# Kernel tuning notes

Hardware: AMD Instinct MI355X
Metric: run time of the kernel (lower is better)

Reference implementation:

```python
import jax, jax.numpy as jnp
import numpy as np

B, FP, ENC, H, V, SEQ = 512, 4096, 64, 512, 42, 128


def _lin(k, out_d, in_d, scale=0.05):
    kw, kb = jax.random.split(k)
    return (jax.random.normal(kw, (out_d, in_d), jnp.float32) * scale,
            jax.random.normal(kb, (out_d,), jnp.float32) * scale)


def setup_inputs() -> dict:
    key = jax.random.key(0)
    ks = jax.random.split(key, 16)
    inp = {}
    inp["X"] = jax.random.normal(ks[0], (B, FP), jnp.float32)
    inp["y"] = jax.random.normal(ks[1], (B, SEQ, V), jnp.float32)
    inp["eps"] = jax.random.normal(ks[2], (B, ENC), jnp.float32)
    inp["e_fc1w"], inp["e_fc1b"] = _lin(ks[3], 2048, FP, 0.02)
    inp["e_fc2w"], inp["e_fc2b"] = _lin(ks[4], 1024, 2048)
    inp["e_fc3w"], inp["e_fc3b"] = _lin(ks[5], 512, 1024)
    inp["e_fc41w"], inp["e_fc41b"] = _lin(ks[6], ENC, 512)
    inp["e_fc42w"], inp["e_fc42b"] = _lin(ks[7], ENC, 512)
    inp["d_fc1w"], inp["d_fc1b"] = _lin(ks[8], H, ENC)
    inp["d_fc2w"], inp["d_fc2b"] = _lin(ks[9], V, H)
    inp["w_ih0"], inp["b_ih0"] = _lin(ks[10], 3 * H, V)
    inp["w_hh0"], inp["b_hh0"] = _lin(ks[11], 3 * H, H)
    inp["w_ih1"], inp["b_ih1"] = _lin(ks[12], 3 * H, H)
    inp["w_hh1"], inp["b_hh1"] = _lin(ks[13], 3 * H, H)
    return inp


def _gru_cell(x, h, w_ih, w_hh, b_ih, b_hh):
    # PyTorch GRU gate math.
    gi = x @ w_ih.T + b_ih  # [B, 3H]
    gh = h @ w_hh.T + b_hh  # [B, 3H]
    ir, iz, i_n = jnp.split(gi, 3, axis=-1)
    hr, hz, h_n = jnp.split(gh, 3, axis=-1)
    r = jax.nn.sigmoid(ir + hr)
    z = jax.nn.sigmoid(iz + hz)
    n = jnp.tanh(i_n + r * h_n)
    return (1.0 - z) * n + z * h


def reference(X, y, eps, e_fc1w, e_fc1b, e_fc2w, e_fc2b, e_fc3w, e_fc3b,
              e_fc41w, e_fc41b, e_fc42w, e_fc42b, d_fc1w, d_fc1b,
              d_fc2w, d_fc2b, w_ih0, b_ih0, w_hh0, b_hh0,
              w_ih1, b_ih1, w_hh1, b_hh1):
    # --- VAE encoder ---
    h1 = jax.nn.relu(X @ e_fc1w.T + e_fc1b)
    h2 = jax.nn.relu(h1 @ e_fc2w.T + e_fc2b)
    h3 = jax.nn.relu(h2 @ e_fc3w.T + e_fc3b)
    mu = h3 @ e_fc41w.T + e_fc41b
    logvar = h3 @ e_fc42w.T + e_fc42b
    kld = jnp.mean(-0.5 * jnp.sum(1.0 + logvar - mu ** 2 - jnp.exp(logvar), axis=1))
    encoded = eps * jnp.exp(0.5 * logvar) + mu  # reparameterize (eps supplied)

    batch = X.shape[0]
    lat = encoded @ d_fc1w.T + d_fc1b  # [B, H]
    hid0 = jnp.zeros((2, batch, H), X.dtype).at[0].set(lat)
    start = jnp.zeros((V,), X.dtype).at[41].set(1.0)
    x0 = jnp.broadcast_to(start, (batch, V))

    def step(carry, _):
        x, hid = carry
        h_l0 = _gru_cell(x, hid[0], w_ih0, w_hh0, b_ih0, b_hh0)
        h_l1 = _gru_cell(h_l0, hid[1], w_ih1, w_hh1, b_ih1, b_hh1)
        out = h_l1 @ d_fc2w.T + d_fc2b  # [B, V]
        return (out, jnp.stack([h_l0, h_l1])), out

    _, outs = jax.lax.scan(step, (x0, hid0), None, length=SEQ)
    decoded = jnp.transpose(outs, (1, 0, 2))  # [B, SEQ, V]
    return decoded, kld
```

## Files before the change

kernel.cpp:

```cpp
#include <hip/hip_runtime.h>
#include <math.h>

constexpr int kB = 512, kENC = 64, kH = 512, kV = 42, kSEQ = 128;
constexpr int kWPitch = 520;
constexpr int kWRows  = 96;
constexpr int kZPad   = kWRows * kWPitch;
constexpr int kCsAByte = (kZPad + 32) * 2;
constexpr int kLdsBytes = kCsAByte + 30720 + 15360;

typedef __attribute__((ext_vector_type(8))) short bf16x8;
typedef __attribute__((ext_vector_type(4))) float f32x4;
typedef unsigned long long u64;

__device__ __forceinline__ unsigned short f2bf(float x) {
  union { float f; unsigned u; } c; c.f = x;
  unsigned r = c.u + 0x7FFFu + ((c.u >> 16) & 1u);
  return (unsigned short)(r >> 16);
}
__device__ __forceinline__ float sigm(float x) { return 1.f / (1.f + expf(-x)); }

__device__ __forceinline__ void ld_row16(const unsigned short* p, bf16x8 (&r)[16]) {
  asm volatile(
    "global_load_dwordx4 %0, %16, off sc0 sc1\n\t"
    "global_load_dwordx4 %1, %16, off offset:64 sc0 sc1\n\t"
    "global_load_dwordx4 %2, %16, off offset:128 sc0 sc1\n\t"
    "global_load_dwordx4 %3, %16, off offset:192 sc0 sc1\n\t"
    "global_load_dwordx4 %4, %16, off offset:256 sc0 sc1\n\t"
    "global_load_dwordx4 %5, %16, off offset:320 sc0 sc1\n\t"
    "global_load_dwordx4 %6, %16, off offset:384 sc0 sc1\n\t"
    "global_load_dwordx4 %7, %16, off offset:448 sc0 sc1\n\t"
    "global_load_dwordx4 %8, %16, off offset:512 sc0 sc1\n\t"
    "global_load_dwordx4 %9, %16, off offset:576 sc0 sc1\n\t"
    "global_load_dwordx4 %10, %16, off offset:640 sc0 sc1\n\t"
    "global_load_dwordx4 %11, %16, off offset:704 sc0 sc1\n\t"
    "global_load_dwordx4 %12, %16, off offset:768 sc0 sc1\n\t"
    "global_load_dwordx4 %13, %16, off offset:832 sc0 sc1\n\t"
    "global_load_dwordx4 %14, %16, off offset:896 sc0 sc1\n\t"
    "global_load_dwordx4 %15, %16, off offset:960 sc0 sc1\n\t"
    "s_waitcnt vmcnt(0)"
    : "=&v"(r[0]), "=&v"(r[1]), "=&v"(r[2]), "=&v"(r[3]),
      "=&v"(r[4]), "=&v"(r[5]), "=&v"(r[6]), "=&v"(r[7]),
      "=&v"(r[8]), "=&v"(r[9]), "=&v"(r[10]), "=&v"(r[11]),
      "=&v"(r[12]), "=&v"(r[13]), "=&v"(r[14]), "=&v"(r[15])
    : "v"(p)
    : "memory");
}

__device__ __forceinline__ void st_h2(unsigned short* p, unsigned short v) {
  __hip_atomic_store(p, v, __ATOMIC_RELAXED, __HIP_MEMORY_SCOPE_AGENT);
}

__device__ __forceinline__ void mg_barrier(unsigned* bar, unsigned ev, int mg, int sub) {
  __syncthreads();
  if (threadIdx.x == 0) {
    const unsigned o = __hip_atomic_fetch_add(&bar[(mg * 8 + sub) * 16], 1u,
        __ATOMIC_RELAXED, __HIP_MEMORY_SCOPE_AGENT);
    if (o == ev * 8u - 1u) {
      const unsigned o2 = __hip_atomic_fetch_add(&bar[(32 + mg) * 16], 1u,
          __ATOMIC_RELAXED, __HIP_MEMORY_SCOPE_AGENT);
      if (o2 == ev * 8u - 1u)
        __hip_atomic_store(&bar[(36 + mg) * 16], ev,
                           __ATOMIC_RELEASE, __HIP_MEMORY_SCOPE_AGENT);
    }
    while (__hip_atomic_load(&bar[(36 + mg) * 16], __ATOMIC_RELAXED,
                             __HIP_MEMORY_SCOPE_AGENT) < ev)
      __builtin_amdgcn_s_sleep(1);
    (void)__hip_atomic_load(&bar[(36 + mg) * 16], __ATOMIC_ACQUIRE,
                            __HIP_MEMORY_SCOPE_AGENT);
  }
  __syncthreads();
}

template<bool RELU>
__global__ __launch_bounds__(256) void gemm_bias(const float* __restrict__ A,
    const float* __restrict__ W, const float* __restrict__ bias,
    float* __restrict__ C, int M, int N, int K)
{
  __shared__ float As[16][68];
  __shared__ float Bs[16][68];
  const int tid = threadIdx.x;
  const int n0 = blockIdx.x * 64;
  const int m0 = blockIdx.y * 64;
  const int tx = tid & 15;
  const int ty = tid >> 4;
  const int lr = tid >> 2;
  const int lk = (tid & 3) << 2;
  float acc[4][4] = {};
  for (int kc = 0; kc < K; kc += 16) {
    const float4 va = *(const float4*)(A + (size_t)(m0 + lr) * K + kc + lk);
    const float4 vb = *(const float4*)(W + (size_t)(n0 + lr) * K + kc + lk);
    __syncthreads();
    As[lk+0][lr] = va.x; As[lk+1][lr] = va.y; As[lk+2][lr] = va.z; As[lk+3][lr] = va.w;
    Bs[lk+0][lr] = vb.x; Bs[lk+1][lr] = vb.y; Bs[lk+2][lr] = vb.z; Bs[lk+3][lr] = vb.w;
    __syncthreads();
#pragma unroll
    for (int k = 0; k < 16; ++k) {
      const float4 a = *(const float4*)&As[k][ty << 2];
      const float4 b = *(const float4*)&Bs[k][tx << 2];
      const float av[4] = {a.x, a.y, a.z, a.w};
      const float bv[4] = {b.x, b.y, b.z, b.w};
#pragma unroll
      for (int i = 0; i < 4; ++i)
#pragma unroll
        for (int jj = 0; jj < 4; ++jj) acc[i][jj] = fmaf(av[i], bv[jj], acc[i][jj]);
    }
  }
  const int cn = n0 + (tx << 2);
  const float4 b4 = *(const float4*)&bias[cn];
  const float bvv[4] = {b4.x, b4.y, b4.z, b4.w};
#pragma unroll
  for (int i = 0; i < 4; ++i) {
    float4 o;
    float* op = &o.x;
#pragma unroll
    for (int jj = 0; jj < 4; ++jj) {
      float v = acc[i][jj] + bvv[jj];
      if (RELU) v = fmaxf(v, 0.f);
      op[jj] = v;
    }
    *(float4*)(C + (size_t)(m0 + (ty << 2) + i) * N + cn) = o;
  }
}

__global__ __launch_bounds__(256) void enc_kld(const float* __restrict__ mu,
    const float* __restrict__ lv, const float* __restrict__ eps,
    float* __restrict__ enc, float* __restrict__ kld)
{
  const int idx = blockIdx.x * 256 + threadIdx.x;
  const float m = mu[idx], l = lv[idx];
  enc[idx] = eps[idx] * expf(0.5f * l) + m;
  float term = 1.0f + l - m * m - expf(l);
  __shared__ float red[256];
  red[threadIdx.x] = term;
  __syncthreads();
  for (int s = 128; s > 0; s >>= 1) {
    if (threadIdx.x < s) red[threadIdx.x] += red[threadIdx.x + s];
    __syncthreads();
  }
  if (threadIdx.x == 0) atomicAdd(kld, -0.5f * red[0] / (float)kB);
}

__global__ __launch_bounds__(256) void prep_comb(const float* __restrict__ wih0,
    const float* __restrict__ bih0, const float* __restrict__ fc2w,
    const float* __restrict__ fc2b, unsigned short* __restrict__ Wcb,
    float* __restrict__ bc, float* __restrict__ g0)
{
  const int idx = blockIdx.x * 256 + threadIdx.x;
  const int n = idx >> 9, j = idx & 511;
  float s = 0.f;
#pragma unroll
  for (int v = 0; v < kV; ++v) s = fmaf(wih0[n * kV + v], fc2w[v * kH + j], s);
  Wcb[idx] = f2bf(s);
  if (j == 0) {
    float sb = 0.f;
    for (int v = 0; v < kV; ++v) sb = fmaf(wih0[n * kV + v], fc2b[v], sb);
    bc[n] = bih0[n] + sb;
  }
  if (j == 1) g0[n] = wih0[n * kV + 41] + bih0[n];
}

__global__ __launch_bounds__(256) void conv_bf16(const float* __restrict__ s,
                                                 unsigned short* __restrict__ d, int n)
{
  const int i = blockIdx.x * 256 + threadIdx.x;
  if (i < n) d[i] = f2bf(s[i]);
}

__global__ __launch_bounds__(256) void conv_fc2w_pad(const float* __restrict__ fc2w,
                                                     unsigned short* __restrict__ d)
{
  const int i = blockIdx.x * 256 + threadIdx.x;
  if (i < 48 * kH) {
    const int r = i >> 9, k = i & 511;
    d[i] = (r < kV) ? f2bf(fc2w[r * kH + k]) : 0;
  }
}

__global__ __launch_bounds__(1024) void gru_mfma(
    const unsigned short* __restrict__ Wcb, const unsigned short* __restrict__ whh0b,
    const unsigned short* __restrict__ wih1b, const unsigned short* __restrict__ whh1b,
    const unsigned short* __restrict__ fc2wb,
    const float* __restrict__ bc, const float* __restrict__ g0,
    const float* __restrict__ bhh0, const float* __restrict__ bih1,
    const float* __restrict__ bhh1, const float* __restrict__ fc2b,
    const float* __restrict__ latg,
    unsigned short* h0A, unsigned short* h0B,
    unsigned short* h1A, unsigned short* h1B,
    float* __restrict__ out, unsigned* bar)
{
  extern __shared__ char smem[];
  unsigned short* w = (unsigned short*)smem;
  float* CsA = (float*)(smem + kCsAByte);
  float* CsB = CsA + 7680;

  const int tid = threadIdx.x;
  const int wave = tid >> 6;
  const int lane = tid & 63;
  const int quad = lane >> 4;
  const int flr  = lane & 15;
  const int q8   = quad * 8;
  const int bid = blockIdx.x;
  const int jg = bid >> 2, mg = bid & 3;
  const int jbase = jg * 8;
  const int m0 = mg * 128;
  const int sub = jg & 7;

  for (int c = tid; c < kWRows * 64; c += 1024) {
    const int row = c >> 6;
    const int k8 = (c & 63) << 3;
    const unsigned short* src;
    int srow;
    if (row < 48) {
      const int g = row >> 4, n = row & 15;
      srow = g * kH + jbase + (n & 7);
      src = (n < 8) ? Wcb : whh1b;
    } else if (row < 72) {
      const int rr = row - 48;
      srow = (rr >> 3) * kH + jbase + (rr & 7);
      src = whh0b;
    } else {
      const int rr = row - 72;
      srow = (rr >> 3) * kH + jbase + (rr & 7);
      src = wih1b;
    }
    *(uint4*)&w[row * kWPitch + k8] = *(const uint4*)&src[(size_t)srow * kH + k8];
  }
  if (tid < 32) w[kZPad + tid] = 0;

  int boffT0[3], boffT1[3], boffB[3];
#pragma unroll
  for (int g = 0; g < 3; ++g) {
    boffT0[g] = (g * 16 + flr) * kWPitch + q8;
    boffT1[g] = (flr < 8) ? (48 + g * 8 + flr) * kWPitch + q8 : kZPad + q8;
    boffB[g]  = (flr < 8) ? (72 + g * 8 + flr) * kWPitch + q8 : kZPad + q8;
  }

  const int gm = tid >> 3;
  const int jl = tid & 7;
  const int gmt = gm >> 4, gml = gm & 15;
  const int j = jbase + jl;

  const float bg0r = g0[j], bg0z = g0[kH + j], bg0n = g0[2 * kH + j];
  const float bbcr = bc[j], bbcz = bc[kH + j], bbcn = bc[2 * kH + j];
  const float bh0r = bhh0[j], bh0z = bhh0[kH + j], bh0n = bhh0[2 * kH + j];
  const float bi1r = bih1[j], bi1z = bih1[kH + j], bi1n = bih1[2 * kH + j];
  const float bh1r = bhh1[j], bh1z = bhh1[kH + j], bh1n = bhh1[2 * kH + j];

  float hp0 = latg[(size_t)(m0 + gm) * kH + j];
  float hp1 = 0.f;

  const bool isProj = (jg < 3) && (wave >= 8);
  const int pv = jg * 16 + flr;
  const float fbv = (isProj && pv < kV) ? fc2b[pv] : 0.f;

  __syncthreads();

  const unsigned short* h0c = h0A; unsigned short* h0n_ = h0B;
  const unsigned short* h1c = h1A; unsigned short* h1n_ = h1B;
  const f32x4 zf = {0.f, 0.f, 0.f, 0.f};

  for (int t = 0; t < kSEQ; ++t) {
    if (wave < 8) {
      const unsigned short* ap = h1c + (size_t)(m0 + wave * 16 + flr) * kH + q8;
      bf16x8 areg[16];
      ld_row16(ap, areg);
      f32x4 acc[3] = {zf, zf, zf};
#pragma unroll
      for (int kf = 0; kf < 16; ++kf) {
        const int ko = kf * 32;
#pragma unroll
        for (int g = 0; g < 3; ++g)
          acc[g] = __builtin_amdgcn_mfma_f32_16x16x32_bf16(
              areg[kf], *(const bf16x8*)&w[boffT0[g] + ko], acc[g], 0, 0, 0);
      }
#pragma unroll
      for (int g = 0; g < 3; ++g)
        *(f32x4*)&CsA[((g * 8 + wave) * 16 + flr) * 20 + quad * 4] = acc[g];
    } else {
      const int mt = wave - 8;
      const unsigned short* ap = h0c + (size_t)(m0 + mt * 16 + flr) * kH + q8;
      bf16x8 areg[16];
      ld_row16(ap, areg);
      f32x4 acc[3] = {zf, zf, zf};
#pragma unroll
      for (int kf = 0; kf < 16; ++kf) {
        const int ko = kf * 32;
#pragma unroll
        for (int g = 0; g < 3; ++g)
          acc[g] = __builtin_amdgcn_mfma_f32_16x16x32_bf16(
              areg[kf], *(const bf16x8*)&w[boffT1[g] + ko], acc[g], 0, 0, 0);
      }
      if (flr < 8) {
#pragma unroll
        for (int g = 0; g < 3; ++g)
          *(f32x4*)&CsB[((g * 8 + mt) * 8 + flr) * 20 + quad * 4] = acc[g];
      }
    }
    __syncthreads();
    {
      const float gir = CsA[((0 * 8 + gmt) * 16 + jl) * 20 + gml] + ((t == 0) ? bg0r : bbcr);
      const float giz = CsA[((1 * 8 + gmt) * 16 + jl) * 20 + gml] + ((t == 0) ? bg0z : bbcz);
      const float gin = CsA[((2 * 8 + gmt) * 16 + jl) * 20 + gml] + ((t == 0) ? bg0n : bbcn);
      const float ghr = CsB[((0 * 8 + gmt) * 8 + jl) * 20 + gml] + bh0r;
      const float ghz = CsB[((1 * 8 + gmt) * 8 + jl) * 20 + gml] + bh0z;
      const float ghn = CsB[((2 * 8 + gmt) * 8 + jl) * 20 + gml] + bh0n;
      const float r = sigm(gir + ghr);
      const float z = sigm(giz + ghz);
      const float n = tanhf(gin + r * ghn);
      const float h = (1.f - z) * n + z * hp0;
      hp0 = h;
      st_h2(h0n_ + (size_t)(m0 + gm) * kH + j, f2bf(h));
    }
    mg_barrier(bar, (unsigned)(2 * t + 1), mg, sub);
    if (wave < 8) {
      const unsigned short* ap = h0n_ + (size_t)(m0 + wave * 16 + flr) * kH + q8;
      bf16x8 areg[16];
      ld_row16(ap, areg);
      f32x4 acc[3] = {zf, zf, zf};
#pragma unroll
      for (int kf = 0; kf < 16; ++kf) {
        const int ko = kf * 32;
#pragma unroll
        for (int g = 0; g < 3; ++g)
          acc[g] = __builtin_amdgcn_mfma_f32_16x16x32_bf16(
              areg[kf], *(const bf16x8*)&w[boffB[g] + ko], acc[g], 0, 0, 0);
      }
      if (flr < 8) {
#pragma unroll
        for (int g = 0; g < 3; ++g)
          *(f32x4*)&CsB[((g * 8 + wave) * 8 + flr) * 20 + quad * 4] = acc[g];
      }
    } else if (isProj && t > 0) {
      const int mt = wave - 8;
      const unsigned short* ap = h1c + (size_t)(m0 + mt * 16 + flr) * kH + q8;
      const unsigned short* bp = fc2wb + (size_t)(jg * 16 + flr) * kH + q8;
      bf16x8 areg[16];
      ld_row16(ap, areg);
      f32x4 pa = zf;
#pragma unroll
      for (int kf = 0; kf < 16; ++kf) {
        const int ko = kf * 32;
        pa = __builtin_amdgcn_mfma_f32_16x16x32_bf16(
            areg[kf], *(const bf16x8*)(bp + ko), pa, 0, 0, 0);
      }
      if (pv < kV) {
#pragma unroll
        for (int r = 0; r < 4; ++r)
          out[(size_t)(m0 + mt * 16 + quad * 4 + r) * (kSEQ * kV)
              + (size_t)(t - 1) * kV + pv] = pa[r] + fbv;
      }
    }
    __syncthreads();
    {
      const float gir = CsB[((0 * 8 + gmt) * 8 + jl) * 20 + gml] + bi1r;
      const float giz = CsB[((1 * 8 + gmt) * 8 + jl) * 20 + gml] + bi1z;
      const float gin = CsB[((2 * 8 + gmt) * 8 + jl) * 20 + gml] + bi1n;
      const float ghr = CsA[((0 * 8 + gmt) * 16 + 8 + jl) * 20 + gml] + bh1r;
      const float ghz = CsA[((1 * 8 + gmt) * 16 + 8 + jl) * 20 + gml] + bh1z;
      const float ghn = CsA[((2 * 8 + gmt) * 16 + 8 + jl) * 20 + gml] + bh1n;
      const float r = sigm(gir + ghr);
      const float z = sigm(giz + ghz);
      const float n = tanhf(gin + r * ghn);
      const float h = (1.f - z) * n + z * hp1;
      hp1 = h;
      st_h2(h1n_ + (size_t)(m0 + gm) * kH + j, f2bf(h));
    }
    mg_barrier(bar, (unsigned)(2 * t + 2), mg, sub);
    {
      const unsigned short* tc;
      tc = h0c; h0c = h0n_; h0n_ = (unsigned short*)tc;
      tc = h1c; h1c = h1n_; h1n_ = (unsigned short*)tc;
    }
  }
  if (isProj) {
    const int mt = wave - 8;
    const unsigned short* ap = h1c + (size_t)(m0 + mt * 16 + flr) * kH + q8;
    const unsigned short* bp = fc2wb + (size_t)(jg * 16 + flr) * kH + q8;
    bf16x8 areg[16];
    ld_row16(ap, areg);
    f32x4 pa = zf;
#pragma unroll
    for (int kf = 0; kf < 16; ++kf) {
      const int ko = kf * 32;
      pa = __builtin_amdgcn_mfma_f32_16x16x32_bf16(
          areg[kf], *(const bf16x8*)(bp + ko), pa, 0, 0, 0);
    }
    if (pv < kV) {
#pragma unroll
      for (int r = 0; r < 4; ++r)
        out[(size_t)(m0 + mt * 16 + quad * 4 + r) * (kSEQ * kV)
            + (size_t)(kSEQ - 1) * kV + pv] = pa[r] + fbv;
    }
  }
}

extern "C" void kernel_launch(void* const* d_in, const int* in_sizes, int n_in,
                              void* d_out, int out_size, void* d_ws, size_t ws_size,
                              hipStream_t stream) {
  const float* X    = (const float*)d_in[0];
  const float* eps  = (const float*)d_in[2];
  const float* e1w  = (const float*)d_in[3];  const float* e1b  = (const float*)d_in[4];
  const float* e2w  = (const float*)d_in[5];  const float* e2b  = (const float*)d_in[6];
  const float* e3w  = (const float*)d_in[7];  const float* e3b  = (const float*)d_in[8];
  const float* e41w = (const float*)d_in[9];  const float* e41b = (const float*)d_in[10];
  const float* e42w = (const float*)d_in[11]; const float* e42b = (const float*)d_in[12];
  const float* fc1w = (const float*)d_in[13]; const float* fc1b = (const float*)d_in[14];
  const float* fc2w = (const float*)d_in[15]; const float* fc2b = (const float*)d_in[16];
  const float* wih0 = (const float*)d_in[17]; const float* bih0 = (const float*)d_in[18];
  const float* whh0 = (const float*)d_in[19]; const float* bhh0 = (const float*)d_in[20];
  const float* wih1 = (const float*)d_in[21]; const float* bih1 = (const float*)d_in[22];
  const float* whh1 = (const float*)d_in[23]; const float* bhh1 = (const float*)d_in[24];
  float* out = (float*)d_out;

  float* ws = (float*)d_ws;
  float* eh1 = ws;
  unsigned short* Wcb   = (unsigned short*)(ws + 0);
  unsigned short* whh0b = (unsigned short*)(ws + 393216);
  unsigned short* fc2wb = (unsigned short*)(ws + 786432);
  float* eh2 = ws + 1048576;
  unsigned short* wih1b = (unsigned short*)(ws + 1048576);
  unsigned short* whh1b = (unsigned short*)(ws + 1441792);
  float* eh3 = ws + 1572864;
  float* latg = ws + 1835008;
  unsigned short* h0a = (unsigned short*)(ws + 2097152);
  unsigned short* h0b = (unsigned short*)(ws + 2228224);
  unsigned short* h1a = (unsigned short*)(ws + 2359296);
  unsigned short* h1b = (unsigned short*)(ws + 2490368);
  float* mu  = ws + 2621440;
  float* lv  = ws + 2654208;
  float* enc = ws + 2686976;
  float* bc  = ws + 2719744;
  float* g0  = ws + 2721280;
  unsigned* bar = (unsigned*)(ws + 2723840);

  const size_t dec_elems = (size_t)kB * kSEQ * kV;

  gemm_bias<true ><<<dim3(32, 8), 256, 0, stream>>>(X,   e1w, e1b, eh1, kB, 2048, 4096);
  gemm_bias<true ><<<dim3(16, 8), 256, 0, stream>>>(eh1, e2w, e2b, eh2, kB, 1024, 2048);
  gemm_bias<true ><<<dim3( 8, 8), 256, 0, stream>>>(eh2, e3w, e3b, eh3, kB,  512, 1024);
  gemm_bias<false><<<dim3( 1, 8), 256, 0, stream>>>(eh3, e41w, e41b, mu, kB,   64,  512);
  gemm_bias<false><<<dim3( 1, 8), 256, 0, stream>>>(eh3, e42w, e42b, lv, kB,   64,  512);
  hipMemsetAsync(out + dec_elems, 0, sizeof(float), stream);
  enc_kld<<<128, 256, 0, stream>>>(mu, lv, eps, enc, out + dec_elems);
  gemm_bias<false><<<dim3(8, 8), 256, 0, stream>>>(enc, fc1w, fc1b, latg, kB, kH, kENC);

  prep_comb<<<3072, 256, 0, stream>>>(wih0, bih0, fc2w, fc2b, Wcb, bc, g0);
  conv_bf16<<<3072, 256, 0, stream>>>(whh0, whh0b, 1536 * kH);
  conv_bf16<<<3072, 256, 0, stream>>>(wih1, wih1b, 1536 * kH);
  conv_bf16<<<3072, 256, 0, stream>>>(whh1, whh1b, 1536 * kH);
  conv_fc2w_pad<<<96, 256, 0, stream>>>(fc2w, fc2wb);
  conv_bf16<<<1024, 256, 0, stream>>>(latg, h0a, kB * kH);
  hipMemsetAsync(h1a, 0, (size_t)kB * kH * sizeof(unsigned short), stream);
  hipMemsetAsync(bar, 0, 4096, stream);

  hipFuncSetAttribute((const void*)gru_mfma,
                      hipFuncAttributeMaxDynamicSharedMemorySize, kLdsBytes);
  void* args[] = { (void*)&Wcb, (void*)&whh0b, (void*)&wih1b, (void*)&whh1b,
                   (void*)&fc2wb, (void*)&bc, (void*)&g0, (void*)&bhh0,
                   (void*)&bih1, (void*)&bhh1, (void*)&fc2b, (void*)&latg,
                   (void*)&h0a, (void*)&h0b, (void*)&h1a, (void*)&h1b,
                   (void*)&out, (void*)&bar };
  hipLaunchCooperativeKernel((void*)gru_mfma, dim3(256), dim3(1024), args,
                             kLdsBytes, stream);
}
```

Before: 4.210 ms.

## Reuse layer-1 h0 fragments across steps and move gate biases to LDS

Swaps the roles of the two wave groups in the first phase so that waves 0-7 reuse the h0 fragments they already loaded for the layer-1 input GEMM as the A operand of the next step's W_hh0 product. This removes one global reload of h0 per step. Waves 8-15 now load h1 for the combined layer-0 input/layer-1 hidden product. The fifteen per-thread bias scalars move into a small LDS table, which frees registers at the cost of extra LDS reads in the gate epilogues.

Measured after the change: 3.708 ms. -11.9%, faster.

```diff
diff --git a/kernel.cpp b/kernel.cpp
--- a/kernel.cpp
+++ b/kernel.cpp
@@ -6,7 +6,7 @@
 constexpr int kWRows  = 96;
 constexpr int kZPad   = kWRows * kWPitch;
 constexpr int kCsAByte = (kZPad + 32) * 2;
-constexpr int kLdsBytes = kCsAByte + 30720 + 15360;
+constexpr int kLdsBytes = kCsAByte + 30720 + 15360 + 480;
 
 typedef __attribute__((ext_vector_type(8))) short bf16x8;
 typedef __attribute__((ext_vector_type(4))) float f32x4;
@@ -192,6 +192,7 @@
   unsigned short* w = (unsigned short*)smem;
   float* CsA = (float*)(smem + kCsAByte);
   float* CsB = CsA + 7680;
+  float* bt  = CsB + 3840;
 
   const int tid = threadIdx.x;
   const int wave = tid >> 6;
@@ -227,6 +228,18 @@
   }
   if (tid < 32) w[kZPad + tid] = 0;
 
+  if (tid < 120) {
+    const int r = tid >> 3, jjl = tid & 7;
+    const int jj = jbase + jjl;
+    float v;
+    if (r < 3)       v = g0[r * kH + jj];
+    else if (r < 6)  v = bc[(r - 3) * kH + jj];
+    else if (r < 9)  v = bhh0[(r - 6) * kH + jj];
+    else if (r < 12) v = bih1[(r - 9) * kH + jj];
+    else             v = bhh1[(r - 12) * kH + jj];
+    bt[tid] = v;
+  }
+
   int boffT0[3], boffT1[3], boffB[3];
 #pragma unroll
   for (int g = 0; g < 3; ++g) {
@@ -240,12 +253,6 @@
   const int gmt = gm >> 4, gml = gm & 15;
   const int j = jbase + jl;
 
-  const float bg0r = g0[j], bg0z = g0[kH + j], bg0n = g0[2 * kH + j];
-  const float bbcr = bc[j], bbcz = bc[kH + j], bbcn = bc[2 * kH + j];
-  const float bh0r = bhh0[j], bh0z = bhh0[kH + j], bh0n = bhh0[2 * kH + j];
-  const float bi1r = bih1[j], bi1z = bih1[kH + j], bi1n = bih1[2 * kH + j];
-  const float bh1r = bhh1[j], bh1z = bhh1[kH + j], bh1n = bhh1[2 * kH + j];
-
   float hp0 = latg[(size_t)(m0 + gm) * kH + j];
   float hp1 = 0.f;
 
@@ -259,11 +266,17 @@
   const unsigned short* h1c = h1A; unsigned short* h1n_ = h1B;
   const f32x4 zf = {0.f, 0.f, 0.f, 0.f};
 
+  bf16x8 ar[16];
+  if (wave < 8) {
+    const unsigned short* ap0 = h0c + (size_t)(m0 + wave * 16 + flr) * kH + q8;
+    ld_row16(ap0, ar);
+  }
+
   for (int t = 0; t < kSEQ; ++t) {
-    if (wave < 8) {
-      const unsigned short* ap = h1c + (size_t)(m0 + wave * 16 + flr) * kH + q8;
-      bf16x8 areg[16];
-      ld_row16(ap, areg);
+    if (wave >= 8) {
+      const int wv = wave - 8;
+      const unsigned short* ap = h1c + (size_t)(m0 + wv * 16 + flr) * kH + q8;
+      ld_row16(ap, ar);
       f32x4 acc[3] = {zf, zf, zf};
 #pragma unroll
       for (int kf = 0; kf < 16; ++kf) {
@@ -271,16 +284,12 @@
 #pragma unroll
         for (int g = 0; g < 3; ++g)
           acc[g] = __builtin_amdgcn_mfma_f32_16x16x32_bf16(
-              areg[kf], *(const bf16x8*)&w[boffT0[g] + ko], acc[g], 0, 0, 0);
+              ar[kf], *(const bf16x8*)&w[boffT0[g] + ko], acc[g], 0, 0, 0);
       }
 #pragma unroll
       for (int g = 0; g < 3; ++g)
-        *(f32x4*)&CsA[((g * 8 + wave) * 16 + flr) * 20 + quad * 4] = acc[g];
+        *(f32x4*)&CsA[((g * 8 + wv) * 16 + flr) * 20 + quad * 4] = acc[g];
     } else {
-      const int mt = wave - 8;
-      const unsigned short* ap = h0c + (size_t)(m0 + mt * 16 + flr) * kH + q8;
-      bf16x8 areg[16];
-      ld_row16(ap, areg);
       f32x4 acc[3] = {zf, zf, zf};
 #pragma unroll
       for (int kf = 0; kf < 16; ++kf) {
@@ -288,22 +297,22 @@
 #pragma unroll
         for (int g = 0; g < 3; ++g)
           acc[g] = __builtin_amdgcn_mfma_f32_16x16x32_bf16(
-              areg[kf], *(const bf16x8*)&w[boffT1[g] + ko], acc[g], 0, 0, 0);
+              ar[kf], *(const bf16x8*)&w[boffT1[g] + ko], acc[g], 0, 0, 0);
       }
       if (flr < 8) {
 #pragma unroll
         for (int g = 0; g < 3; ++g)
-          *(f32x4*)&CsB[((g * 8 + mt) * 8 + flr) * 20 + quad * 4] = acc[g];
+          *(f32x4*)&CsB[((g * 8 + wave) * 8 + flr) * 20 + quad * 4] = acc[g];
       }
     }
     __syncthreads();
     {
-      const float gir = CsA[((0 * 8 + gmt) * 16 + jl) * 20 + gml] + ((t == 0) ? bg0r : bbcr);
-      const float giz = CsA[((1 * 8 + gmt) * 16 + jl) * 20 + gml] + ((t == 0) ? bg0z : bbcz);
-      const float gin = CsA[((2 * 8 + gmt) * 16 + jl) * 20 + gml] + ((t == 0) ? bg0n : bbcn);
-      const float ghr = CsB[((0 * 8 + gmt) * 8 + jl) * 20 + gml] + bh0r;
-      const float ghz = CsB[((1 * 8 + gmt) * 8 + jl) * 20 + gml] + bh0z;
-      const float ghn = CsB[((2 * 8 + gmt) * 8 + jl) * 20 + gml] + bh0n;
+      const float gir = CsA[((0 * 8 + gmt) * 16 + jl) * 20 + gml] + bt[(t == 0 ? 0 : 3) * 8 + jl];
+      const float giz = CsA[((1 * 8 + gmt) * 16 + jl) * 20 + gml] + bt[(t == 0 ? 1 : 4) * 8 + jl];
+      const float gin = CsA[((2 * 8 + gmt) * 16 + jl) * 20 + gml] + bt[(t == 0 ? 2 : 5) * 8 + jl];
+      const float ghr = CsB[((0 * 8 + gmt) * 8 + jl) * 20 + gml] + bt[6 * 8 + jl];
+      const float ghz = CsB[((1 * 8 + gmt) * 8 + jl) * 20 + gml] + bt[7 * 8 + jl];
+      const float ghn = CsB[((2 * 8 + gmt) * 8 + jl) * 20 + gml] + bt[8 * 8 + jl];
       const float r = sigm(gir + ghr);
       const float z = sigm(giz + ghz);
       const float n = tanhf(gin + r * ghn);
@@ -314,8 +323,7 @@
     mg_barrier(bar, (unsigned)(2 * t + 1), mg, sub);
     if (wave < 8) {
       const unsigned short* ap = h0n_ + (size_t)(m0 + wave * 16 + flr) * kH + q8;
-      bf16x8 areg[16];
-      ld_row16(ap, areg);
+      ld_row16(ap, ar);
       f32x4 acc[3] = {zf, zf, zf};
 #pragma unroll
       for (int kf = 0; kf < 16; ++kf) {
@@ -323,7 +331,7 @@
 #pragma unroll
         for (int g = 0; g < 3; ++g)
           acc[g] = __builtin_amdgcn_mfma_f32_16x16x32_bf16(
-              areg[kf], *(const bf16x8*)&w[boffB[g] + ko], acc[g], 0, 0, 0);
+              ar[kf], *(const bf16x8*)&w[boffB[g] + ko], acc[g], 0, 0, 0);
       }
       if (flr < 8) {
 #pragma unroll
@@ -334,14 +342,13 @@
       const int mt = wave - 8;
       const unsigned short* ap = h1c + (size_t)(m0 + mt * 16 + flr) * kH + q8;
       const unsigned short* bp = fc2wb + (size_t)(jg * 16 + flr) * kH + q8;
-      bf16x8 areg[16];
-      ld_row16(ap, areg);
+      ld_row16(ap, ar);
       f32x4 pa = zf;
 #pragma unroll
       for (int kf = 0; kf < 16; ++kf) {
         const int ko = kf * 32;
         pa = __builtin_amdgcn_mfma_f32_16x16x32_bf16(
-            areg[kf], *(const bf16x8*)(bp + ko), pa, 0, 0, 0);
+            ar[kf], *(const bf16x8*)(bp + ko), pa, 0, 0, 0);
       }
       if (pv < kV) {
 #pragma unroll
@@ -352,12 +359,12 @@
     }
     __syncthreads();
     {
-      const float gir = CsB[((0 * 8 + gmt) * 8 + jl) * 20 + gml] + bi1r;
-      const float giz = CsB[((1 * 8 + gmt) * 8 + jl) * 20 + gml] + bi1z;
-      const float gin = CsB[((2 * 8 + gmt) * 8 + jl) * 20 + gml] + bi1n;
-      const float ghr = CsA[((0 * 8 + gmt) * 16 + 8 + jl) * 20 + gml] + bh1r;
-      const float ghz = CsA[((1 * 8 + gmt) * 16 + 8 + jl) * 20 + gml] + bh1z;
-      const float ghn = CsA[((2 * 8 + gmt) * 16 + 8 + jl) * 20 + gml] + bh1n;
+      const float gir = CsB[((0 * 8 + gmt) * 8 + jl) * 20 + gml] + bt[9 * 8 + jl];
+      const float giz = CsB[((1 * 8 + gmt) * 8 + jl) * 20 + gml] + bt[10 * 8 + jl];
+      const float gin = CsB[((2 * 8 + gmt) * 8 + jl) * 20 + gml] + bt[11 * 8 + jl];
+      const float ghr = CsA[((0 * 8 + gmt) * 16 + 8 + jl) * 20 + gml] + bt[12 * 8 + jl];
+      const float ghz = CsA[((1 * 8 + gmt) * 16 + 8 + jl) * 20 + gml] + bt[13 * 8 + jl];
+      const float ghn = CsA[((2 * 8 + gmt) * 16 + 8 + jl) * 20 + gml] + bt[14 * 8 + jl];
       const float r = sigm(gir + ghr);
       const float z = sigm(giz + ghz);
       const float n = tanhf(gin + r * ghn);
@@ -376,14 +383,13 @@
     const int mt = wave - 8;
     const unsigned short* ap = h1c + (size_t)(m0 + mt * 16 + flr) * kH + q8;
     const unsigned short* bp = fc2wb + (size_t)(jg * 16 + flr) * kH + q8;
-    bf16x8 areg[16];
-    ld_row16(ap, areg);
+    ld_row16(ap, ar);
     f32x4 pa = zf;
 #pragma unroll
     for (int kf = 0; kf < 16; ++kf) {
       const int ko = kf * 32;
       pa = __builtin_amdgcn_mfma_f32_16x16x32_bf16(
-          areg[kf], *(const bf16x8*)(bp + ko), pa, 0, 0, 0);
+          ar[kf], *(const bf16x8*)(bp + ko), pa, 0, 0, 0);
     }
     if (pv < kV) {
 #pragma unroll
```
